# Performance work log

Hardware: AMD Instinct MI355X
Metric: run time of the kernel (lower is better)

Reference implementation:

```python
import jax, jax.numpy as jnp
import numpy as np

N_NODES = 50000

def setup_inputs() -> dict:
    key = jax.random.key(0)
    k1, k2, k3, k4, k5 = jax.random.split(key, 5)
    feat = jax.random.normal(k1, (N_NODES, 192), dtype=jnp.float32)
    edge_feat = jax.random.normal(k2, (800000, 64), dtype=jnp.float32)
    src = jax.random.randint(k3, (800000,), 0, N_NODES, dtype=jnp.int32)
    dst = jax.random.randint(k4, (800000,), 0, N_NODES, dtype=jnp.int32)
    weight = jax.random.normal(k5, (256, 256), dtype=jnp.float32) * (1.0 / np.sqrt(256.0))
    bias = jnp.zeros((256,), dtype=jnp.float32)
    return {"feat": feat, "edge_feat": edge_feat, "src": src, "dst": dst,
            "weight": weight, "bias": bias}


def reference(feat, edge_feat, src, dst, weight, bias):
    N = feat.shape[0]
    ones_e = jnp.ones(src.shape[0], dtype=jnp.float32)
    # out-degree normalization of source features (pre-aggregation)
    out_deg = jnp.clip(jax.ops.segment_sum(ones_e, src, num_segments=N), 1.0, None)
    feat_n = feat * (out_deg ** -0.5)[:, None]            # [N, d_node]
    # message = concat(src_feat_norm, edge_feat); sum over dst.
    # segment_sum distributes over concat, so aggregate parts separately
    # (avoids materializing the [E, d_node+d_edge] message tensor).
    h_src = jax.ops.segment_sum(feat_n[src], dst, num_segments=N)   # [N, d_node]
    h_edge = jax.ops.segment_sum(edge_feat, dst, num_segments=N)    # [N, d_edge]
    h = jnp.concatenate([h_src, h_edge], axis=1)          # [N, in_feats]
    rst = h @ weight                                      # [N, out_feats]
    # in-degree normalization (post-aggregation)
    in_deg = jnp.clip(jax.ops.segment_sum(ones_e, dst, num_segments=N), 1.0, None)
    rst = rst * (in_deg ** -0.5)[:, None] + bias
    return rst
```

## Files before the change

kernel.cpp:

```cpp
#include <hip/hip_runtime.h>

#define NN 50000
#define NE 800000
#define DIN 256
#define DOUT 256

#define LDS_STRIDE 264

typedef __attribute__((ext_vector_type(8))) short bf16x8;
typedef __attribute__((ext_vector_type(8))) unsigned short u16x8;
typedef __attribute__((ext_vector_type(4))) float f32x4;

__device__ __forceinline__ unsigned short f2bf(float x) {
    unsigned int u = __builtin_bit_cast(unsigned int, x);
    u += 0x7fffu + ((u >> 16) & 1u);
    return (unsigned short)(u >> 16);
}
__device__ __forceinline__ float bf2f(unsigned short b) {
    return __builtin_bit_cast(float, ((unsigned int)b) << 16);
}


__global__ __launch_bounds__(256) void zero_meta(int* __restrict__ p, int n) {
    int i = blockIdx.x * 256 + threadIdx.x;
    if (i < n) p[i] = 0;
}

__global__ __launch_bounds__(256) void count_kernel(const int* __restrict__ src,
                                                    const int* __restrict__ dst,
                                                    int* __restrict__ in_cnt,
                                                    int* __restrict__ out_cnt) {
    int e = blockIdx.x * 256 + threadIdx.x;
    if (e < NE) {
        atomicAdd(in_cnt + dst[e], 1);
        atomicAdd(out_cnt + src[e], 1);
    }
}

__global__ __launch_bounds__(256) void scan1(const int* __restrict__ cnt,
                                             int* __restrict__ row_off,
                                             int* __restrict__ bsum) {
    __shared__ int tmp[256];
    int tid = threadIdx.x;
    int i = blockIdx.x * 256 + tid;
    int v = (i < NN) ? cnt[i] : 0;
    tmp[tid] = v;
    __syncthreads();
#pragma unroll
    for (int off = 1; off < 256; off <<= 1) {
        int t = (tid >= off) ? tmp[tid - off] : 0;
        __syncthreads();
        if (tid >= off) tmp[tid] += t;
        __syncthreads();
    }
    if (i < NN) row_off[i] = tmp[tid] - v;
    if (tid == 255) bsum[blockIdx.x] = tmp[255];
}

__global__ __launch_bounds__(256) void scan2(int* __restrict__ bsum, int nb) {
    __shared__ int tmp[256];
    int tid = threadIdx.x;
    int v = (tid < nb) ? bsum[tid] : 0;
    tmp[tid] = v;
    __syncthreads();
#pragma unroll
    for (int off = 1; off < 256; off <<= 1) {
        int t = (tid >= off) ? tmp[tid - off] : 0;
        __syncthreads();
        if (tid >= off) tmp[tid] += t;
        __syncthreads();
    }
    if (tid < nb) bsum[tid] = tmp[tid] - v;
}

__global__ __launch_bounds__(256) void scan3(int* __restrict__ row_off,
                                             int* __restrict__ cursor,
                                             float* __restrict__ odeg_inv,
                                             const int* __restrict__ out_cnt,
                                             const int* __restrict__ bsum) {
    int i = blockIdx.x * 256 + threadIdx.x;
    if (i < NN) {
        int v = row_off[i] + bsum[i >> 8];
        row_off[i] = v;
        cursor[i] = v;
        odeg_inv[i] = rsqrtf((float)max(out_cnt[i], 1));
    }
    if (i == NN) row_off[NN] = NE;
}

__global__ __launch_bounds__(256) void wconv(const float* __restrict__ W,
                                             unsigned short* __restrict__ wt) {
    int n = blockIdx.x, k = threadIdx.x;
    wt[n * 256 + k] = f2bf(W[k * 256 + n]);
}

__global__ __launch_bounds__(256) void featconv(const float* __restrict__ feat,
                                                const float* __restrict__ odeg_inv,
                                                unsigned short* __restrict__ featn) {
    int node = blockIdx.x * 4 + (threadIdx.x >> 6);
    int lane = threadIdx.x & 63;
    if (node >= NN || lane >= 48) return;
    float s = odeg_inv[node];
    float4 v = *(const float4*)(feat + (size_t)node * 192 + lane * 4);
    ushort4 o;
    o.x = f2bf(v.x * s); o.y = f2bf(v.y * s);
    o.z = f2bf(v.z * s); o.w = f2bf(v.w * s);
    *(ushort4*)(featn + (size_t)node * 192 + lane * 4) = o;
}

__global__ __launch_bounds__(256) void fill_kernel(const int* __restrict__ src,
                                                   const int* __restrict__ dst,
                                                   int* __restrict__ cursor,
                                                   int* __restrict__ perm,
                                                   unsigned short* __restrict__ eperm,
                                                   const float* __restrict__ edge_feat) {
    int tid = threadIdx.x;
    int e   = blockIdx.x * 16 + (tid >> 4);
    int sub = tid & 15;
    if (e >= NE) return;
    int pos = 0;
    if (sub == 0) {
        pos = atomicAdd(cursor + dst[e], 1);
        perm[pos] = src[e];
    }
    pos = __shfl(pos, 0, 16);
    float4 v = *(const float4*)(edge_feat + (size_t)e * 64 + sub * 4);
    ushort4 o;
    o.x = f2bf(v.x); o.y = f2bf(v.y); o.z = f2bf(v.z); o.w = f2bf(v.w);
    *(ushort4*)(eperm + (size_t)pos * 64 + sub * 4) = o;
}

__global__ __launch_bounds__(256) void agg_gemm(const unsigned short* __restrict__ featn,
                                                const unsigned short* __restrict__ eperm,
                                                const int* __restrict__ row_off,
                                                const int* __restrict__ perm,
                                                const unsigned short* __restrict__ wt_bf,
                                                const float* __restrict__ bias,
                                                float* __restrict__ out) {
    __shared__ unsigned short hlds[16 * LDS_STRIDE];

    int wave = threadIdx.x >> 6;
    int lane = threadIdx.x & 63;
    int rbase = blockIdx.x * 16;

    int half = lane >> 5;
    int l    = lane & 31;
    bool isF = (l < 24);
    const unsigned short* fbase = featn + l * 8;
    const unsigned short* ebase = eperm + (l - 24) * 8;

    for (int c = 0; c < 4; ++c) {
        int node = rbase + wave * 4 + c;
        int start = row_off[node];
        int end   = row_off[node + 1];

        float acc[8];
#pragma unroll
        for (int k = 0; k < 8; ++k) acc[k] = 0.f;

        for (int i = start + half; i < end; i += 8) {
            int idx[4]; float w[4]; int s[4];
#pragma unroll
            for (int j = 0; j < 4; ++j) {
                int ii = i + 2 * j;
                idx[j] = min(ii, end - 1);
                w[j] = (ii < end) ? 1.f : 0.f;
            }
#pragma unroll
            for (int j = 0; j < 4; ++j) s[j] = perm[idx[j]];
            bf16x8 u[4];
#pragma unroll
            for (int j = 0; j < 4; ++j) {
                const unsigned short* p = isF ? (fbase + (size_t)s[j] * 192)
                                              : (ebase + (size_t)idx[j] * 64);
                u[j] = *(const bf16x8*)p;
            }
#pragma unroll
            for (int j = 0; j < 4; ++j) {
#pragma unroll
                for (int k = 0; k < 8; ++k)
                    acc[k] = fmaf(bf2f((unsigned short)u[j][k]), w[j], acc[k]);
            }
        }

#pragma unroll
        for (int k = 0; k < 8; ++k) acc[k] += __shfl_xor(acc[k], 32);

        if (lane < 32) {
            u16x8 o;
#pragma unroll
            for (int k = 0; k < 8; ++k) o[k] = f2bf(acc[k]);
            *(u16x8*)(hlds + (wave * 4 + c) * LDS_STRIDE + l * 8) = o;
        }
    }

    __syncthreads();

    int m16  = lane & 15;
    int quad = lane >> 4;
    int cbase = wave * 64;

    const unsigned short* arow = hlds + m16 * LDS_STRIDE + quad * 8;
    const unsigned short* b0p = wt_bf + (size_t)(cbase +  0 + m16) * 256 + quad * 8;
    const unsigned short* b1p = wt_bf + (size_t)(cbase + 16 + m16) * 256 + quad * 8;
    const unsigned short* b2p = wt_bf + (size_t)(cbase + 32 + m16) * 256 + quad * 8;
    const unsigned short* b3p = wt_bf + (size_t)(cbase + 48 + m16) * 256 + quad * 8;

    f32x4 acc0 = {0.f, 0.f, 0.f, 0.f};
    f32x4 acc1 = {0.f, 0.f, 0.f, 0.f};
    f32x4 acc2 = {0.f, 0.f, 0.f, 0.f};
    f32x4 acc3 = {0.f, 0.f, 0.f, 0.f};

#pragma unroll
    for (int k0 = 0; k0 < 256; k0 += 32) {
        bf16x8 a  = *(const bf16x8*)(arow + k0);
        bf16x8 b0 = *(const bf16x8*)(b0p + k0);
        bf16x8 b1 = *(const bf16x8*)(b1p + k0);
        bf16x8 b2 = *(const bf16x8*)(b2p + k0);
        bf16x8 b3 = *(const bf16x8*)(b3p + k0);
        acc0 = __builtin_amdgcn_mfma_f32_16x16x32_bf16(a, b0, acc0, 0, 0, 0);
        acc1 = __builtin_amdgcn_mfma_f32_16x16x32_bf16(a, b1, acc1, 0, 0, 0);
        acc2 = __builtin_amdgcn_mfma_f32_16x16x32_bf16(a, b2, acc2, 0, 0, 0);
        acc3 = __builtin_amdgcn_mfma_f32_16x16x32_bf16(a, b3, acc3, 0, 0, 0);
    }

    int grow0 = rbase + quad * 4;
    float s[4];
    int ro_prev = row_off[grow0];
#pragma unroll
    for (int r = 0; r < 4; ++r) {
        int nx = row_off[grow0 + r + 1];
        s[r] = rsqrtf((float)max(nx - ro_prev, 1));
        ro_prev = nx;
    }

    float bv0 = bias[cbase +  0 + m16];
    float bv1 = bias[cbase + 16 + m16];
    float bv2 = bias[cbase + 32 + m16];
    float bv3 = bias[cbase + 48 + m16];

#pragma unroll
    for (int r = 0; r < 4; ++r) {
        size_t rowoff = (size_t)(grow0 + r) * DOUT;
        out[rowoff + cbase +  0 + m16] = acc0[r] * s[r] + bv0;
        out[rowoff + cbase + 16 + m16] = acc1[r] * s[r] + bv1;
        out[rowoff + cbase + 32 + m16] = acc2[r] * s[r] + bv2;
        out[rowoff + cbase + 48 + m16] = acc3[r] * s[r] + bv3;
    }
}

__global__ __launch_bounds__(256) void fill_fb(const int* __restrict__ src,
                                               const int* __restrict__ dst,
                                               int* __restrict__ cursor,
                                               int2* __restrict__ perm2) {
    int e = blockIdx.x * 256 + threadIdx.x;
    if (e < NE) {
        int d = dst[e];
        int pos = atomicAdd(cursor + d, 1);
        perm2[pos] = make_int2(e, src[e]);
    }
}

__global__ __launch_bounds__(256) void aggregate_fb(const unsigned short* __restrict__ featn,
                                                    const float* __restrict__ edge_feat,
                                                    const int* __restrict__ row_off,
                                                    const int2* __restrict__ perm2,
                                                    unsigned short* __restrict__ h_bf) {
    int node = blockIdx.x * 4 + (threadIdx.x >> 6);
    int lane = threadIdx.x & 63;
    if (node >= NN) return;
    int start = row_off[node];
    int end   = row_off[node + 1];

    float4 acc = make_float4(0.f, 0.f, 0.f, 0.f);

    if (lane < 48) {
        const unsigned short* fb = featn + lane * 4;
        for (int i = start; i < end; i += 8) {
            int2 p[8];
#pragma unroll
            for (int j = 0; j < 8; ++j) p[j] = perm2[min(i + j, end - 1)];
            ushort4 u[8];
#pragma unroll
            for (int j = 0; j < 8; ++j)
                u[j] = *(const ushort4*)(fb + (size_t)p[j].y * 192);
#pragma unroll
            for (int j = 0; j < 8; ++j) {
                float w = (i + j < end) ? 1.f : 0.f;
                acc.x = fmaf(bf2f(u[j].x), w, acc.x);
                acc.y = fmaf(bf2f(u[j].y), w, acc.y);
                acc.z = fmaf(bf2f(u[j].z), w, acc.z);
                acc.w = fmaf(bf2f(u[j].w), w, acc.w);
            }
        }
    } else {
        const float* eb = edge_feat + (lane - 48) * 4;
        for (int i = start; i < end; i += 8) {
            int2 p[8];
#pragma unroll
            for (int j = 0; j < 8; ++j) p[j] = perm2[min(i + j, end - 1)];
            float4 v[8];
#pragma unroll
            for (int j = 0; j < 8; ++j)
                v[j] = *(const float4*)(eb + (size_t)p[j].x * 64);
#pragma unroll
            for (int j = 0; j < 8; ++j) {
                float w = (i + j < end) ? 1.f : 0.f;
                acc.x = fmaf(v[j].x, w, acc.x);
                acc.y = fmaf(v[j].y, w, acc.y);
                acc.z = fmaf(v[j].z, w, acc.z);
                acc.w = fmaf(v[j].w, w, acc.w);
            }
        }
    }

    ushort4 o;
    o.x = f2bf(acc.x); o.y = f2bf(acc.y);
    o.z = f2bf(acc.z); o.w = f2bf(acc.w);
    *(ushort4*)(h_bf + (size_t)node * 256 + lane * 4) = o;
}

__global__ __launch_bounds__(256) void gemm_mfma(const unsigned short* __restrict__ h_bf,
                                                 const unsigned short* __restrict__ wt_bf,
                                                 const float* __restrict__ bias,
                                                 const int* __restrict__ row_off,
                                                 float* __restrict__ out) {
    int wave = threadIdx.x >> 6;
    int lane = threadIdx.x & 63;
    int m16  = lane & 15;
    int quad = lane >> 4;
    int rbase = blockIdx.x * 16;
    int cbase = wave * 64;

    const unsigned short* arow = h_bf + (size_t)(rbase + m16) * 256 + quad * 8;
    const unsigned short* b0p = wt_bf + (size_t)(cbase +  0 + m16) * 256 + quad * 8;
    const unsigned short* b1p = wt_bf + (size_t)(cbase + 16 + m16) * 256 + quad * 8;
    const unsigned short* b2p = wt_bf + (size_t)(cbase + 32 + m16) * 256 + quad * 8;
    const unsigned short* b3p = wt_bf + (size_t)(cbase + 48 + m16) * 256 + quad * 8;

    f32x4 acc0 = {0.f, 0.f, 0.f, 0.f};
    f32x4 acc1 = {0.f, 0.f, 0.f, 0.f};
    f32x4 acc2 = {0.f, 0.f, 0.f, 0.f};
    f32x4 acc3 = {0.f, 0.f, 0.f, 0.f};

#pragma unroll
    for (int k0 = 0; k0 < 256; k0 += 32) {
        bf16x8 a  = *(const bf16x8*)(arow + k0);
        bf16x8 b0 = *(const bf16x8*)(b0p + k0);
        bf16x8 b1 = *(const bf16x8*)(b1p + k0);
        bf16x8 b2 = *(const bf16x8*)(b2p + k0);
        bf16x8 b3 = *(const bf16x8*)(b3p + k0);
        acc0 = __builtin_amdgcn_mfma_f32_16x16x32_bf16(a, b0, acc0, 0, 0, 0);
        acc1 = __builtin_amdgcn_mfma_f32_16x16x32_bf16(a, b1, acc1, 0, 0, 0);
        acc2 = __builtin_amdgcn_mfma_f32_16x16x32_bf16(a, b2, acc2, 0, 0, 0);
        acc3 = __builtin_amdgcn_mfma_f32_16x16x32_bf16(a, b3, acc3, 0, 0, 0);
    }

    int grow0 = rbase + quad * 4;
    float s[4];
    int ro_prev = row_off[grow0];
#pragma unroll
    for (int r = 0; r < 4; ++r) {
        int nx = row_off[grow0 + r + 1];
        s[r] = rsqrtf((float)max(nx - ro_prev, 1));
        ro_prev = nx;
    }

    float bv0 = bias[cbase +  0 + m16];
    float bv1 = bias[cbase + 16 + m16];
    float bv2 = bias[cbase + 32 + m16];
    float bv3 = bias[cbase + 48 + m16];

#pragma unroll
    for (int r = 0; r < 4; ++r) {
        size_t rowoff = (size_t)(grow0 + r) * DOUT;
        out[rowoff + cbase +  0 + m16] = acc0[r] * s[r] + bv0;
        out[rowoff + cbase + 16 + m16] = acc1[r] * s[r] + bv1;
        out[rowoff + cbase + 32 + m16] = acc2[r] * s[r] + bv2;
        out[rowoff + cbase + 48 + m16] = acc3[r] * s[r] + bv3;
    }
}

extern "C" void kernel_launch(void* const* d_in, const int* in_sizes, int n_in,
                              void* d_out, int out_size, void* d_ws, size_t ws_size,
                              hipStream_t stream) {
    const float* feat      = (const float*)d_in[0];
    const float* edge_feat = (const float*)d_in[1];
    const int*   src       = (const int*)d_in[2];
    const int*   dst       = (const int*)d_in[3];
    const float* W         = (const float*)d_in[4];
    const float* bias      = (const float*)d_in[5];
    float* out = (float*)d_out;

    unsigned short* h_bf  = (unsigned short*)d_ws;
    unsigned short* wt_bf = h_bf + (size_t)NN * DIN;
    unsigned short* featn = wt_bf + 256 * 256;

    unsigned short* eperm = featn + (size_t)NN * 192;
    int*   perm_b     = (int*)(eperm + (size_t)NE * 64);
    int*   row_off_b  = perm_b + NE;
    float* odeg_inv_b = (float*)(row_off_b + NN + 2);
    int*   cursor_b   = (int*)(odeg_inv_b + NN);
    int*   bsum_b     = cursor_b + NN;
    size_t need = (size_t)((char*)(bsum_b + 256) - (char*)d_ws);

    int*   row_off_s  = (int*)(featn + (size_t)NN * 192);
    float* odeg_inv_s = (float*)(row_off_s + NN + 2);
    int*   cursor_s   = (int*)(odeg_inv_s + NN);
    int*   bsum_s     = cursor_s + NN;
    int2*  perm2      = (int2*)(bsum_s + 256);

    bool big_ws = (ws_size >= need);

    int*   row_off  = big_ws ? row_off_b  : row_off_s;
    float* odeg_inv = big_ws ? odeg_inv_b : odeg_inv_s;
    int*   cursor   = big_ws ? cursor_b   : cursor_s;
    int*   bsum     = big_ws ? bsum_b     : bsum_s;
    int*   in_cnt   = big_ws ? perm_b     : (int*)perm2;
    int*   out_cnt  = in_cnt + NN;

    const int SCAN_BLOCKS = (NN + 255) / 256;

    zero_meta<<<(2 * NN + 255) / 256, 256, 0, stream>>>(in_cnt, 2 * NN);
    count_kernel<<<(NE + 255) / 256, 256, 0, stream>>>(src, dst, in_cnt, out_cnt);
    scan1<<<SCAN_BLOCKS, 256, 0, stream>>>(in_cnt, row_off, bsum);
    scan2<<<1, 256, 0, stream>>>(bsum, SCAN_BLOCKS);
    scan3<<<(NN + 256) / 256, 256, 0, stream>>>(row_off, cursor, odeg_inv, out_cnt, bsum);
    wconv<<<256, 256, 0, stream>>>(W, wt_bf);
    if (big_ws) {
        fill_kernel<<<NE / 16, 256, 0, stream>>>(src, dst, cursor, perm_b,
                                                 eperm, edge_feat);
        featconv<<<(NN + 3) / 4, 256, 0, stream>>>(feat, odeg_inv, featn);
        agg_gemm<<<NN / 16, 256, 0, stream>>>(featn, eperm, row_off, perm_b,
                                              wt_bf, bias, out);
    } else {
        featconv<<<(NN + 3) / 4, 256, 0, stream>>>(feat, odeg_inv, featn);
        fill_fb<<<(NE + 255) / 256, 256, 0, stream>>>(src, dst, cursor, perm2);
        aggregate_fb<<<(NN + 3) / 4, 256, 0, stream>>>(featn, edge_feat, row_off,
                                                       perm2, h_bf);
        gemm_mfma<<<NN / 16, 256, 0, stream>>>(h_bf, wt_bf, bias, row_off, out);
    }
}
```

Measured before the change: 536.9 us.

## Gather four destination nodes concurrently per wave in the aggregate-GEMM kernel

Before, each wave walked its four destination nodes one after another, issuing four gathers per step for a single node. Now the wave handles all four nodes in one loop, running to the largest degree among them, with two edges per half-wave per node. That puts eight independent gathers in flight per step and aims to hide memory latency on the irregular feature loads. In exchange it keeps four accumulator sets live, raising register pressure, and wastes masked loads when the four nodes' degrees differ.

```diff
diff --git a/kernel.cpp b/kernel.cpp
--- a/kernel.cpp
+++ b/kernel.cpp
@@ -149,49 +149,78 @@
     const unsigned short* fbase = featn + l * 8;
     const unsigned short* ebase = eperm + (l - 24) * 8;
 
+    int pos[4], end4[4];
+    int nsteps = 0;
+#pragma unroll
     for (int c = 0; c < 4; ++c) {
         int node = rbase + wave * 4 + c;
-        int start = row_off[node];
-        int end   = row_off[node + 1];
-
-        float acc[8];
-#pragma unroll
-        for (int k = 0; k < 8; ++k) acc[k] = 0.f;
-
-        for (int i = start + half; i < end; i += 8) {
-            int idx[4]; float w[4]; int s[4];
-#pragma unroll
-            for (int j = 0; j < 4; ++j) {
-                int ii = i + 2 * j;
-                idx[j] = min(ii, end - 1);
-                w[j] = (ii < end) ? 1.f : 0.f;
+        int st = row_off[node];
+        end4[c] = row_off[node + 1];
+        pos[c] = st + half;
+        int deg = end4[c] - st;
+        nsteps = max(nsteps, (deg + 3) >> 2);
+    }
+
+    float acc0[8], acc1[8], acc2[8], acc3[8];
+#pragma unroll
+    for (int k = 0; k < 8; ++k) { acc0[k] = 0.f; acc1[k] = 0.f; acc2[k] = 0.f; acc3[k] = 0.f; }
+
+    for (int step = 0; step < nsteps; ++step) {
+        int idx[8]; float w[8];
+#pragma unroll
+        for (int c = 0; c < 4; ++c) {
+#pragma unroll
+            for (int j = 0; j < 2; ++j) {
+                int ii = pos[c] + 2 * j;
+                int t = min(ii, end4[c] - 1);
+                t = max(t, 0);
+                idx[c * 2 + j] = t;
+                w[c * 2 + j] = (ii < end4[c]) ? 1.f : 0.f;
             }
-#pragma unroll
-            for (int j = 0; j < 4; ++j) s[j] = perm[idx[j]];
-            bf16x8 u[4];
-#pragma unroll
-            for (int j = 0; j < 4; ++j) {
-                const unsigned short* p = isF ? (fbase + (size_t)s[j] * 192)
-                                              : (ebase + (size_t)idx[j] * 64);
-                u[j] = *(const bf16x8*)p;
+        }
+        int s[8];
+#pragma unroll
+        for (int m = 0; m < 8; ++m) s[m] = perm[idx[m]];
+        bf16x8 u[8];
+#pragma unroll
+        for (int m = 0; m < 8; ++m) {
+            const unsigned short* p = isF ? (fbase + (size_t)s[m] * 192)
+                                          : (ebase + (size_t)idx[m] * 64);
+            u[m] = *(const bf16x8*)p;
+        }
+#pragma unroll
+        for (int j = 0; j < 2; ++j) {
+#pragma unroll
+            for (int k = 0; k < 8; ++k) {
+                acc0[k] = fmaf(bf2f((unsigned short)u[0 + j][k]), w[0 + j], acc0[k]);
+                acc1[k] = fmaf(bf2f((unsigned short)u[2 + j][k]), w[2 + j], acc1[k]);
+                acc2[k] = fmaf(bf2f((unsigned short)u[4 + j][k]), w[4 + j], acc2[k]);
+                acc3[k] = fmaf(bf2f((unsigned short)u[6 + j][k]), w[6 + j], acc3[k]);
             }
-#pragma unroll
-            for (int j = 0; j < 4; ++j) {
-#pragma unroll
-                for (int k = 0; k < 8; ++k)
-                    acc[k] = fmaf(bf2f((unsigned short)u[j][k]), w[j], acc[k]);
-            }
-        }
-
-#pragma unroll
-        for (int k = 0; k < 8; ++k) acc[k] += __shfl_xor(acc[k], 32);
-
-        if (lane < 32) {
-            u16x8 o;
-#pragma unroll
-            for (int k = 0; k < 8; ++k) o[k] = f2bf(acc[k]);
-            *(u16x8*)(hlds + (wave * 4 + c) * LDS_STRIDE + l * 8) = o;
-        }
+        }
+#pragma unroll
+        for (int c = 0; c < 4; ++c) pos[c] += 4;
+    }
+
+#pragma unroll
+    for (int k = 0; k < 8; ++k) {
+        acc0[k] += __shfl_xor(acc0[k], 32);
+        acc1[k] += __shfl_xor(acc1[k], 32);
+        acc2[k] += __shfl_xor(acc2[k], 32);
+        acc3[k] += __shfl_xor(acc3[k], 32);
+    }
+    if (lane < 32) {
+        u16x8 o0, o1, o2, o3;
+#pragma unroll
+        for (int k = 0; k < 8; ++k) {
+            o0[k] = f2bf(acc0[k]); o1[k] = f2bf(acc1[k]);
+            o2[k] = f2bf(acc2[k]); o3[k] = f2bf(acc3[k]);
+        }
+        unsigned short* hb = hlds + wave * 4 * LDS_STRIDE + l * 8;
+        *(u16x8*)(hb + 0 * LDS_STRIDE) = o0;
+        *(u16x8*)(hb + 1 * LDS_STRIDE) = o1;
+        *(u16x8*)(hb + 2 * LDS_STRIDE) = o2;
+        *(u16x8*)(hb + 3 * LDS_STRIDE) = o3;
     }
 
     __syncthreads();
@@ -206,10 +235,10 @@
     const unsigned short* b2p = wt_bf + (size_t)(cbase + 32 + m16) * 256 + quad * 8;
     const unsigned short* b3p = wt_bf + (size_t)(cbase + 48 + m16) * 256 + quad * 8;
 
-    f32x4 acc0 = {0.f, 0.f, 0.f, 0.f};
-    f32x4 acc1 = {0.f, 0.f, 0.f, 0.f};
-    f32x4 acc2 = {0.f, 0.f, 0.f, 0.f};
-    f32x4 acc3 = {0.f, 0.f, 0.f, 0.f};
+    f32x4 acc0v = {0.f, 0.f, 0.f, 0.f};
+    f32x4 acc1v = {0.f, 0.f, 0.f, 0.f};
+    f32x4 acc2v = {0.f, 0.f, 0.f, 0.f};
+    f32x4 acc3v = {0.f, 0.f, 0.f, 0.f};
 
 #pragma unroll
     for (int k0 = 0; k0 < 256; k0 += 32) {
@@ -218,19 +247,19 @@
         bf16x8 b1 = *(const bf16x8*)(b1p + k0);
         bf16x8 b2 = *(const bf16x8*)(b2p + k0);
         bf16x8 b3 = *(const bf16x8*)(b3p + k0);
-        acc0 = __builtin_amdgcn_mfma_f32_16x16x32_bf16(a, b0, acc0, 0, 0, 0);
-        acc1 = __builtin_amdgcn_mfma_f32_16x16x32_bf16(a, b1, acc1, 0, 0, 0);
-        acc2 = __builtin_amdgcn_mfma_f32_16x16x32_bf16(a, b2, acc2, 0, 0, 0);
-        acc3 = __builtin_amdgcn_mfma_f32_16x16x32_bf16(a, b3, acc3, 0, 0, 0);
+        acc0v = __builtin_amdgcn_mfma_f32_16x16x32_bf16(a, b0, acc0v, 0, 0, 0);
+        acc1v = __builtin_amdgcn_mfma_f32_16x16x32_bf16(a, b1, acc1v, 0, 0, 0);
+        acc2v = __builtin_amdgcn_mfma_f32_16x16x32_bf16(a, b2, acc2v, 0, 0, 0);
+        acc3v = __builtin_amdgcn_mfma_f32_16x16x32_bf16(a, b3, acc3v, 0, 0, 0);
     }
 
     int grow0 = rbase + quad * 4;
-    float s[4];
+    float s4[4];
     int ro_prev = row_off[grow0];
 #pragma unroll
     for (int r = 0; r < 4; ++r) {
         int nx = row_off[grow0 + r + 1];
-        s[r] = rsqrtf((float)max(nx - ro_prev, 1));
+        s4[r] = rsqrtf((float)max(nx - ro_prev, 1));
         ro_prev = nx;
     }
 
@@ -242,10 +271,10 @@
 #pragma unroll
     for (int r = 0; r < 4; ++r) {
         size_t rowoff = (size_t)(grow0 + r) * DOUT;
-        out[rowoff + cbase +  0 + m16] = acc0[r] * s[r] + bv0;
-        out[rowoff + cbase + 16 + m16] = acc1[r] * s[r] + bv1;
-        out[rowoff + cbase + 32 + m16] = acc2[r] * s[r] + bv2;
-        out[rowoff + cbase + 48 + m16] = acc3[r] * s[r] + bv3;
+        out[rowoff + cbase +  0 + m16] = acc0v[r] * s4[r] + bv0;
+        out[rowoff + cbase + 16 + m16] = acc1v[r] * s4[r] + bv1;
+        out[rowoff + cbase + 32 + m16] = acc2v[r] * s4[r] + bv2;
+        out[rowoff + cbase + 48 + m16] = acc3v[r] * s4[r] + bv3;
     }
 }
 
```

New measurement: 536.0 us. No clear change (-0.2%).
